# Performance work log

Hardware: AMD Instinct MI355X
Metric: run time of the kernel (lower is better)

The kernel has to match this reference:

```python
import jax, jax.numpy as jnp
import numpy as np

N_QUBITS = 8
IN_DIM = 256
HID = 8  # must equal N_QUBITS (broadcasting in the original cell requires it)
B = 512
T = 512


def _zmat(n):
    # [2^n, n] matrix of Pauli-Z eigenvalues per basis state / wire (wire 0 = MSB,
    # matching torchquantum's state ordering).
    idx = np.arange(2 ** n)
    bits = (idx[:, None] >> (n - 1 - np.arange(n))) & 1
    return jnp.asarray(1.0 - 2.0 * bits, dtype=jnp.float32)


def _apply_rx(state, theta, w):
    # state: [M, 2, ..., 2] complex64, theta: [M] real. RX(theta) on wire w.
    st = jnp.moveaxis(state, w + 1, 1)
    a0, a1 = st[:, 0], st[:, 1]
    shp = (-1,) + (1,) * (a0.ndim - 1)
    c = jnp.cos(theta * 0.5).reshape(shp).astype(state.dtype)
    s = (-1j * jnp.sin(theta * 0.5)).reshape(shp).astype(state.dtype)
    new = jnp.stack([c * a0 + s * a1, s * a0 + c * a1], axis=1)
    return jnp.moveaxis(new, 1, w + 1)


def _cnot(state, c, t):
    # CNOT control c, target t on state [M, 2, ..., 2].
    s0 = jax.lax.index_in_dim(state, 0, axis=c + 1, keepdims=False)
    s1 = jax.lax.index_in_dim(state, 1, axis=c + 1, keepdims=False)
    t_ax = t + 1 if t < c else t  # target axis index after control axis removed
    s1 = jnp.flip(s1, axis=t_ax)
    return jnp.stack([s0, s1], axis=c + 1)


def _circuit(angles, zmat):
    # angles: [M, n] combined RX angles (encoder x + trainable theta, RX angles add).
    # Returns PauliZ expectation per wire: [M, n].
    M, n = angles.shape
    state = jnp.zeros((M,) + (2,) * n, dtype=jnp.complex64)
    state = state.at[(slice(None),) + (0,) * n].set(1.0 + 0j)
    for w in range(n):
        state = _apply_rx(state, angles[:, w], w)
    for w in range(n - 1):
        state = _cnot(state, w, w + 1)
    state = _cnot(state, n - 1, 0)
    sr = state.reshape(M, -1)
    probs = sr.real ** 2 + sr.imag ** 2  # smooth |amp|^2
    return probs @ zmat


def setup_inputs():
    key = jax.random.key(0)
    ks = jax.random.split(key, 10)
    d = IN_DIM + HID
    sc = 1.0 / np.sqrt(d)
    inp = {"inputs": jax.random.normal(ks[0], (B, T, IN_DIM), dtype=jnp.float32)}
    for i, name in enumerate(["f", "i", "g", "o"]):
        inp["W" + name] = jax.random.uniform(ks[1 + 2 * i], (N_QUBITS, d), minval=-sc, maxval=sc, dtype=jnp.float32)
        inp["b" + name] = jax.random.uniform(ks[2 + 2 * i], (N_QUBITS,), minval=-sc, maxval=sc, dtype=jnp.float32)
    inp["thetas"] = jax.random.normal(ks[9], (4, N_QUBITS), dtype=jnp.float32) * 0.1
    return inp


def reference(inputs, Wf, bf, Wi, bi, Wg, bg, Wo, bo, thetas):
    zmat = _zmat(N_QUBITS)
    bsz = inputs.shape[0]
    hx0 = jnp.zeros((bsz, HID), inputs.dtype)
    cx0 = jnp.zeros((bsz, HID), inputs.dtype)
    W = jnp.stack([Wf, Wi, Wg, Wo])       # [4, n, d]
    bias = jnp.stack([bf, bi, bg, bo])    # [4, n]

    def step(carry, x_t):
        hx, cx = carry
        comb = jnp.concatenate([x_t, hx], axis=1)  # [B, D+H]
        # fc angles + trainable RX angle (RX rotations on same wire compose additively)
        ang = jnp.einsum('gnd,bd->gbn', W, comb) + bias[:, None, :] + thetas[:, None, :]
        m = _circuit(ang.reshape(4 * bsz, N_QUBITS), zmat).reshape(4, bsz, N_QUBITS)
        f = jax.nn.sigmoid(m[0])
        i = jax.nn.sigmoid(m[1])
        g = jnp.tanh(m[2])
        o = jax.nn.sigmoid(m[3])
        cx2 = f * cx + i * g
        hx2 = o * jnp.tanh(cx2)
        return (hx2, cx2), hx2

    (hx, cx), outs = jax.lax.scan(step, (hx0, cx0), jnp.swapaxes(inputs, 0, 1))
    return jnp.swapaxes(outs, 0, 1), hx, cx
```

## Files before the change

### kernel.cpp

```cpp
#include <hip/hip_runtime.h>


#define BQ   512
#define TT   512
#define IND  256
#define PRE_OFF 8704


__global__ void prep_kernel(const float* __restrict__ Wf, const float* __restrict__ bf,
                            const float* __restrict__ Wi, const float* __restrict__ bi,
                            const float* __restrict__ Wg, const float* __restrict__ bg,
                            const float* __restrict__ Wo, const float* __restrict__ bo,
                            const float* __restrict__ th, float* __restrict__ wsf) {
    const float* W[4]    = {Wf, Wi, Wg, Wo};
    const float* bias[4] = {bf, bi, bg, bo};
    int d = threadIdx.x;
    for (int g = 0; g < 4; g++)
        for (int n = 0; n < 8; n++)
            wsf[d * 32 + g * 8 + n] = W[g][n * 264 + d];
    if (d < 32) {
        int g = d >> 3, n = d & 7;
        for (int j = 0; j < 8; j++)
            wsf[8192 + d * 8 + j] = W[g][n * 264 + 256 + j];
        wsf[8448 + d] = bias[g][n] + th[d];
    }
}

__global__ __launch_bounds__(256) void pre_gemm(const float* __restrict__ x,
                                                const float* __restrict__ wsf,
                                                float* __restrict__ pre) {
    const int bt = blockIdx.x * 256 + threadIdx.x;
    const float4* xr = (const float4*)(x + (size_t)bt * IND);
    const float* cvec = wsf + 8448;
    float acc[32];
#pragma unroll
    for (int k = 0; k < 32; k++) acc[k] = cvec[k];
    for (int dq = 0; dq < 64; dq++) {
        float4 xv = xr[dq];
        const float* wr = wsf + dq * 128;
#pragma unroll
        for (int k = 0; k < 32; k++) acc[k] = fmaf(xv.x, wr[k], acc[k]);
#pragma unroll
        for (int k = 0; k < 32; k++) acc[k] = fmaf(xv.y, wr[32 + k], acc[k]);
#pragma unroll
        for (int k = 0; k < 32; k++) acc[k] = fmaf(xv.z, wr[64 + k], acc[k]);
#pragma unroll
        for (int k = 0; k < 32; k++) acc[k] = fmaf(xv.w, wr[96 + k], acc[k]);
    }
    const int b = bt >> 9, t = bt & 511, t4 = t >> 2, tm = t & 3;
    float* dst = pre + ((size_t)(b * 128 + t4)) * 128 + tm;
#pragma unroll
    for (int k = 0; k < 32; k++) dst[k * 4] = acc[k];
}

#define SWZ(x, imm) __int_as_float(__builtin_amdgcn_ds_swizzle(__float_as_int(x), (imm)))

template <int CTRL>
__device__ __forceinline__ float dpp_shr(float x) {
    return __int_as_float(__builtin_amdgcn_update_dpp(
        0, __float_as_int(x), CTRL, 0xF, 0xF, true));
}

__global__ __launch_bounds__(64) void recur(const float* __restrict__ wsf,
                                            float* __restrict__ out) {
    const int lane = threadIdx.x;
    const int l32  = lane & 31;
    const int half = lane >> 5;
    const int b    = blockIdx.x * 2 + half;
    const int g    = l32 >> 3;
    const int n    = l32 & 7;

    float whr[8];
#pragma unroll
    for (int j = 0; j < 8; j++) whr[j] = wsf[8192 + l32 * 8 + j];

    const float4* pp = (const float4*)(wsf + PRE_OFF) + (size_t)b * 128 * 32 + l32;

    float hx[8];
#pragma unroll
    for (int j = 0; j < 8; j++) hx[j] = 0.0f;
    float cx = 0.0f;

    float4 bufA = pp[0];
    float4 bufB = pp[32];

    float* outp = out + (size_t)b * TT * 8 + n;
    const float L2E = 1.4426950408889634f;

    for (int t4 = 0; t4 < 128; t4++) {
        float4 cur = (t4 & 1) ? bufB : bufA;
        int nx = (t4 + 2 < 128) ? (t4 + 2) : 127;
        if (t4 & 1) bufB = pp[(size_t)nx * 32];
        else        bufA = pp[(size_t)nx * 32];
        float pv4[4] = {cur.x, cur.y, cur.z, cur.w};
#pragma unroll
        for (int tm = 0; tm < 4; tm++) {
            float ang = pv4[tm];
#pragma unroll
            for (int j = 0; j < 8; j++) ang = fmaf(whr[j], hx[j], ang);
            float c = __cosf(ang);
            float s = (n == 0) ? 1.0f : c;
            { float v = dpp_shr<0x111>(s); s = (n >= 1) ? s * v : s; }
            { float v = dpp_shr<0x112>(s); s = (n >= 2) ? s * v : s; }
            { float v = dpp_shr<0x114>(s); s = (n >= 4) ? s * v : s; }
            float c0 = SWZ(c, 0x018);
            float s7 = SWZ(s, 0x0F8);
            float m  = (n == 0) ? s7 : c0 * s;
            float kk  = (g == 2) ? (-2.0f * L2E) : (-L2E);
            float u   = __builtin_amdgcn_rcpf(1.0f + __builtin_amdgcn_exp2f(m * kk));
            float val = (g == 2) ? fmaf(2.0f, u, -1.0f) : u;
            float fv = SWZ(val, 0x007);
            float iv = SWZ(val, 0x107);
            float gv = SWZ(val, 0x207);
            float ov = SWZ(val, 0x307);
            cx = fmaf(fv, cx, iv * gv);
            float t2 = __builtin_amdgcn_exp2f(cx * (-2.0f * L2E));
            float th = fmaf(2.0f, __builtin_amdgcn_rcpf(1.0f + t2), -1.0f);
            float hxn = ov * th;
            if (l32 < 8) outp[(t4 * 4 + tm) * 8] = hxn;
            hx[0] = SWZ(hxn, 0x018);
            hx[1] = SWZ(hxn, 0x038);
            hx[2] = SWZ(hxn, 0x058);
            hx[3] = SWZ(hxn, 0x078);
            hx[4] = SWZ(hxn, 0x098);
            hx[5] = SWZ(hxn, 0x0B8);
            hx[6] = SWZ(hxn, 0x0D8);
            hx[7] = SWZ(hxn, 0x0F8);
        }
    }
    if (l32 < 8) {
        out[(size_t)BQ * TT * 8 + b * 8 + n]            = hx[n];
        out[(size_t)BQ * TT * 8 + BQ * 8 + b * 8 + n]   = cx;
    }
}

extern "C" void kernel_launch(void* const* d_in, const int* in_sizes, int n_in,
                              void* d_out, int out_size, void* d_ws, size_t ws_size,
                              hipStream_t stream) {
    const float* x  = (const float*)d_in[0];
    const float* Wf = (const float*)d_in[1];
    const float* bf = (const float*)d_in[2];
    const float* Wi = (const float*)d_in[3];
    const float* bi = (const float*)d_in[4];
    const float* Wg = (const float*)d_in[5];
    const float* bg = (const float*)d_in[6];
    const float* Wo = (const float*)d_in[7];
    const float* bo = (const float*)d_in[8];
    const float* th = (const float*)d_in[9];
    float* wsf = (float*)d_ws;
    float* out = (float*)d_out;

    prep_kernel<<<1, 256, 0, stream>>>(Wf, bf, Wi, bi, Wg, bg, Wo, bo, th, wsf);
    pre_gemm<<<(BQ * TT) / 256, 256, 0, stream>>>(x, wsf, wsf + PRE_OFF);
    recur<<<BQ / 2, 64, 0, stream>>>(wsf, out);
}
```

Measured before the change: 550.1 us.

## Stage input rows through padded LDS tiles with register prefetch in pre_gemm

Each thread previously read its own 1KB input row with strided float4 loads, so a wavefront touched addresses 1KB apart and global accesses were poorly coalesced. The kernel now loads 32-column chunks of 256 rows cooperatively with coalesced float4 loads and writes them to a padded shared-memory tile (stride 33 to avoid bank conflicts). The next chunk is prefetched into registers while the current one is consumed. The cost is two barriers per chunk, scalar LDS reads, and extra register pressure from the 8 float4 prefetch registers on top of 32 accumulators.

```diff
diff --git a/kernel.cpp b/kernel.cpp
--- a/kernel.cpp
+++ b/kernel.cpp
@@ -26,27 +26,64 @@
     }
 }
 
-__global__ __launch_bounds__(256) void pre_gemm(const float* __restrict__ x,
-                                                const float* __restrict__ wsf,
-                                                float* __restrict__ pre) {
-    const int bt = blockIdx.x * 256 + threadIdx.x;
-    const float4* xr = (const float4*)(x + (size_t)bt * IND);
+
+#define ROWS 256
+#define KC   32
+#define NCH  (IND / KC)
+#define LSTR 33
+
+__global__ __launch_bounds__(256, 4) void pre_gemm(const float* __restrict__ x,
+                                                   const float* __restrict__ wsf,
+                                                   float* __restrict__ pre) {
+    __shared__ float tile[ROWS * LSTR];
+    const int tid  = threadIdx.x;
+    const int row0 = blockIdx.x * ROWS;
+
     const float* cvec = wsf + 8448;
     float acc[32];
 #pragma unroll
     for (int k = 0; k < 32; k++) acc[k] = cvec[k];
-    for (int dq = 0; dq < 64; dq++) {
-        float4 xv = xr[dq];
-        const float* wr = wsf + dq * 128;
+
+    float4 R[8];
 #pragma unroll
-        for (int k = 0; k < 32; k++) acc[k] = fmaf(xv.x, wr[k], acc[k]);
+    for (int it = 0; it < 8; it++) {
+        int linear = it * 256 + tid;
+        int srow = linear >> 3, sk4 = linear & 7;
+        R[it] = *(const float4*)(x + (size_t)(row0 + srow) * IND + sk4 * 4);
+    }
+
+#pragma unroll 1
+    for (int c = 0; c < NCH; c++) {
+        __syncthreads();
 #pragma unroll
-        for (int k = 0; k < 32; k++) acc[k] = fmaf(xv.y, wr[32 + k], acc[k]);
+        for (int it = 0; it < 8; it++) {
+            int linear = it * 256 + tid;
+            int srow = linear >> 3, sk4 = linear & 7;
+            float* d = tile + srow * LSTR + sk4 * 4;
+            d[0] = R[it].x; d[1] = R[it].y; d[2] = R[it].z; d[3] = R[it].w;
+        }
+        if (c + 1 < NCH) {
 #pragma unroll
-        for (int k = 0; k < 32; k++) acc[k] = fmaf(xv.z, wr[64 + k], acc[k]);
+            for (int it = 0; it < 8; it++) {
+                int linear = it * 256 + tid;
+                int srow = linear >> 3, sk4 = linear & 7;
+                R[it] = *(const float4*)(x + (size_t)(row0 + srow) * IND
+                                           + (c + 1) * KC + sk4 * 4);
+            }
+        }
+        __syncthreads();
+        const float* xr = tile + tid * LSTR;
+        const float* wb = wsf + c * KC * 32;
 #pragma unroll
-        for (int k = 0; k < 32; k++) acc[k] = fmaf(xv.w, wr[96 + k], acc[k]);
+        for (int k = 0; k < KC; k++) {
+            float xk = xr[k];
+            const float* wr = wb + k * 32;
+#pragma unroll
+            for (int kk = 0; kk < 32; kk++) acc[kk] = fmaf(xk, wr[kk], acc[kk]);
+        }
     }
+
+    const int bt = row0 + tid;
     const int b = bt >> 9, t = bt & 511, t4 = t >> 2, tm = t & 3;
     float* dst = pre + ((size_t)(b * 128 + t4)) * 128 + tm;
 #pragma unroll
```

After: 521.5 us. 5.2% less time.

## Stage pre-GEMM weights in LDS and double-buffer input rows in registers

Applied to the files above, without the earlier changes.

The input-projection kernel now copies the 32KB transposed weight matrix into shared memory once per block, so the inner FMA loop reads broadcast weights from LDS instead of through scalar/global loads. Each thread's input row is loaded in 32-float chunks into two register buffers that alternate, so global loads for the next chunk are issued while the current chunk is consumed. The 32KB of shared memory and the extra registers constrain occupancy, and launch bounds now request 3 blocks per CU.

```diff
diff --git a/kernel.cpp b/kernel.cpp
--- a/kernel.cpp
+++ b/kernel.cpp
@@ -26,27 +26,84 @@
     }
 }
 
-__global__ __launch_bounds__(256) void pre_gemm(const float* __restrict__ x,
-                                                const float* __restrict__ wsf,
-                                                float* __restrict__ pre) {
-    const int bt = blockIdx.x * 256 + threadIdx.x;
-    const float4* xr = (const float4*)(x + (size_t)bt * IND);
+
+#define ROWS 256
+
+__global__ __launch_bounds__(256, 3) void pre_gemm(const float* __restrict__ x,
+                                                   const float* __restrict__ wsf,
+                                                   float* __restrict__ pre) {
+    __shared__ float wlds[8192];
+    const int tid = threadIdx.x;
+
+#pragma unroll
+    for (int i = 0; i < 8; i++) {
+        int i4 = i * 256 + tid;
+        *(float4*)(wlds + (size_t)i4 * 4) = *(const float4*)(wsf + (size_t)i4 * 4);
+    }
+
+    const int row = blockIdx.x * ROWS + tid;
+    const float* xr = x + (size_t)row * IND;
+
+    float acc[32];
     const float* cvec = wsf + 8448;
-    float acc[32];
 #pragma unroll
     for (int k = 0; k < 32; k++) acc[k] = cvec[k];
-    for (int dq = 0; dq < 64; dq++) {
-        float4 xv = xr[dq];
-        const float* wr = wsf + dq * 128;
-#pragma unroll
-        for (int k = 0; k < 32; k++) acc[k] = fmaf(xv.x, wr[k], acc[k]);
-#pragma unroll
-        for (int k = 0; k < 32; k++) acc[k] = fmaf(xv.y, wr[32 + k], acc[k]);
-#pragma unroll
-        for (int k = 0; k < 32; k++) acc[k] = fmaf(xv.z, wr[64 + k], acc[k]);
-#pragma unroll
-        for (int k = 0; k < 32; k++) acc[k] = fmaf(xv.w, wr[96 + k], acc[k]);
-    }
+
+    __syncthreads();
+
+    float4 RA[8], RB[8];
+#pragma unroll
+    for (int j = 0; j < 8; j++) RA[j] = *(const float4*)(xr + j * 4);
+#pragma unroll
+    for (int j = 0; j < 8; j++) RB[j] = *(const float4*)(xr + 32 + j * 4);
+
+#pragma unroll 1
+    for (int bb = 0; bb < 4; bb++) {
+        {
+            const float* wb = wlds + (bb * 64) * 32;
+#pragma unroll
+            for (int j = 0; j < 8; j++) {
+                float4 xv = RA[j];
+                const float* wr = wb + j * 128;
+#pragma unroll
+                for (int kk = 0; kk < 32; kk++) acc[kk] = fmaf(xv.x, wr[kk], acc[kk]);
+#pragma unroll
+                for (int kk = 0; kk < 32; kk++) acc[kk] = fmaf(xv.y, wr[32 + kk], acc[kk]);
+#pragma unroll
+                for (int kk = 0; kk < 32; kk++) acc[kk] = fmaf(xv.z, wr[64 + kk], acc[kk]);
+#pragma unroll
+                for (int kk = 0; kk < 32; kk++) acc[kk] = fmaf(xv.w, wr[96 + kk], acc[kk]);
+            }
+        }
+        {
+            int nb = (2 * bb + 2 < 8) ? (2 * bb + 2) : 7;
+#pragma unroll
+            for (int j = 0; j < 8; j++) RA[j] = *(const float4*)(xr + nb * 32 + j * 4);
+        }
+        {
+            const float* wb = wlds + (bb * 64 + 32) * 32;
+#pragma unroll
+            for (int j = 0; j < 8; j++) {
+                float4 xv = RB[j];
+                const float* wr = wb + j * 128;
+#pragma unroll
+                for (int kk = 0; kk < 32; kk++) acc[kk] = fmaf(xv.x, wr[kk], acc[kk]);
+#pragma unroll
+                for (int kk = 0; kk < 32; kk++) acc[kk] = fmaf(xv.y, wr[32 + kk], acc[kk]);
+#pragma unroll
+                for (int kk = 0; kk < 32; kk++) acc[kk] = fmaf(xv.z, wr[64 + kk], acc[kk]);
+#pragma unroll
+                for (int kk = 0; kk < 32; kk++) acc[kk] = fmaf(xv.w, wr[96 + kk], acc[kk]);
+            }
+        }
+        {
+            int nb = (2 * bb + 3 < 8) ? (2 * bb + 3) : 7;
+#pragma unroll
+            for (int j = 0; j < 8; j++) RB[j] = *(const float4*)(xr + nb * 32 + j * 4);
+        }
+    }
+
+    const int bt = row;
     const int b = bt >> 9, t = bt & 511, t4 = t >> 2, tm = t & 3;
     float* dst = pre + ((size_t)(b * 128 + t4)) * 128 + tm;
 #pragma unroll
```

Measured after the change: 557.0 us. No clear change (+1.2%).
